# Performance work log

Measured on AMD Instinct MI355X. Metric: run time of the kernel, lower is better.

The kernel has to match this reference:

```python
import jax, jax.numpy as jnp
import numpy as np

N = 50000
E = 1600000
IN_C, H1, H2 = 512, 512, 256
N_CLASSES = 40
CENTER_NUM = 8
D_CAT = 2 * H2  # 512


def setup_inputs() -> dict:
    key = jax.random.key(0)
    ks = jax.random.split(key, 9)
    x = jax.random.normal(ks[0], (N, IN_C), dtype=jnp.float32)
    edge_index = jax.random.randint(ks[1], (2, E), 0, N, dtype=jnp.int64)
    s1 = 1.0 / np.sqrt(IN_C)
    s2 = 1.0 / np.sqrt(H1)
    sp = 1.0 / np.sqrt(D_CAT)
    W1 = jax.random.uniform(ks[2], (IN_C, H1), jnp.float32, -s1, s1)
    b1 = jnp.zeros((H1,), jnp.float32)
    W2 = jax.random.uniform(ks[3], (H1, H2), jnp.float32, -s2, s2)
    b2 = jnp.zeros((H2,), jnp.float32)
    Wp = jax.random.uniform(ks[4], (CENTER_NUM, D_CAT), jnp.float32, -sp, sp)   # interior_prototype weight [C, D]
    We = jax.random.uniform(ks[5], (CENTER_NUM, N_CLASSES, D_CAT), jnp.float32, -sp, sp)  # border prototypes
    return {"x": x, "edge_index": edge_index, "W1": W1, "b1": b1, "W2": W2, "b2": b2, "Wp": Wp, "We": We}


def _gcn_conv(x, W, b, src, dst, n):
    # PyG GCNConv: h = xW; out[i] = sum_j norm_ij h[j] + b, with self-loops,
    # norm_ij = deg_i^{-1/2} deg_j^{-1/2}, deg includes self-loop.
    h = x @ W
    ones = jnp.ones(src.shape[0], x.dtype)
    deg = jax.ops.segment_sum(ones, dst, num_segments=n) + 1.0
    dinv = deg ** -0.5
    norm = dinv[src] * dinv[dst]
    agg = jax.ops.segment_sum(h[src] * norm[:, None], dst, num_segments=n)
    agg = agg + h * (dinv * dinv)[:, None]  # self-loop term
    return agg + b


def _mean_aggr(x, src, dst, n):
    # PyG default message x_j with aggr='mean' (custom message_func kwarg is ignored by PyG)
    cnt = jax.ops.segment_sum(jnp.ones(src.shape[0], x.dtype), dst, num_segments=n)
    s = jax.ops.segment_sum(x[src], dst, num_segments=n)
    return s / jnp.maximum(cnt, 1.0)[:, None]


def reference(x, edge_index, W1, b1, W2, b2, Wp, We):
    src, dst = edge_index[0], edge_index[1]
    n = x.shape[0]
    h = jax.nn.relu(_gcn_conv(x, W1, b1, src, dst, n))
    h = _gcn_conv(h, W2, b2, src, dst, n)
    neighbor = _mean_aggr(h, src, dst, n)
    xc = jnp.concatenate([h, neighbor], axis=1)  # [N, 2*H2]
    scores = xc @ Wp.T                            # [N, C]
    idx = jnp.argmax(scores, axis=1)              # [N]
    # all-expert logits then per-node select (same math as masked per-cluster linear)
    all_out = jnp.einsum('nd,ckd->nck', xc, We)   # [N, C, n_classes]
    out = jnp.take_along_axis(all_out, idx[:, None, None], axis=1)[:, 0, :]
    return out, xc
```

## Files before the change

### kernel.cpp

```cpp
#include <hip/hip_runtime.h>
#include <hip/hip_bf16.h>
#include <hip/hip_fp16.h>
#include <cstdint>
#include <cstddef>


using short8 = __attribute__((ext_vector_type(8))) short;
using half8  = __attribute__((ext_vector_type(8))) _Float16;
using f32x4  = __attribute__((ext_vector_type(4))) float;

#define GLB_AS __attribute__((address_space(1)))
#define LDS_AS __attribute__((address_space(3)))

__global__ __launch_bounds__(256) void prep_kernel(
    const float* __restrict__ x, char* __restrict__ xq, float* __restrict__ scale,
    const float* __restrict__ W1, __half* __restrict__ W1T,
    const float* __restrict__ W2, __half* __restrict__ W2T,
    const float* __restrict__ We, __half* __restrict__ We_h,
    int* __restrict__ bcur, int* __restrict__ ecur,
    int n, int nbuck, int cap) {
    const int t = threadIdx.x;
    int b = blockIdx.x;
    const int BXQ = (n + 3) / 4;
    const int BW1 = (512 * 512) / 256;
    const int BW2 = (512 * 256) / 256;
    const int BWe = (8 * 40 * 512) / 256;
    if (b < BXQ) {
        const int node = b * 4 + (t >> 6);
        const int lane = t & 63;
        if (node < n) {
            const float* row = x + (size_t)node * 512;
            const float4 v0 = *(const float4*)&row[lane * 8];
            const float4 v1 = *(const float4*)&row[lane * 8 + 4];
            float m = fmaxf(fmaxf(fmaxf(fabsf(v0.x), fabsf(v0.y)), fmaxf(fabsf(v0.z), fabsf(v0.w))),
                            fmaxf(fmaxf(fabsf(v1.x), fabsf(v1.y)), fmaxf(fabsf(v1.z), fabsf(v1.w))));
#pragma unroll
            for (int off = 32; off; off >>= 1) m = fmaxf(m, __shfl_xor(m, off));
            m = fmaxf(m, 1e-30f);
            const float qs = 127.f / m;
            int q0 = __float2int_rn(v0.x * qs), q1 = __float2int_rn(v0.y * qs);
            int q2 = __float2int_rn(v0.z * qs), q3 = __float2int_rn(v0.w * qs);
            int q4 = __float2int_rn(v1.x * qs), q5 = __float2int_rn(v1.y * qs);
            int q6 = __float2int_rn(v1.z * qs), q7 = __float2int_rn(v1.w * qs);
            uint2 pk;
            pk.x = (q0 & 0xff) | ((q1 & 0xff) << 8) | ((q2 & 0xff) << 16) | ((q3 & 0xff) << 24);
            pk.y = (q4 & 0xff) | ((q5 & 0xff) << 8) | ((q6 & 0xff) << 16) | ((q7 & 0xff) << 24);
            *(uint2*)&xq[(size_t)node * 512 + lane * 8] = pk;
            if (lane == 0) scale[node] = m / 127.f;
        }
        return;
    }
    b -= BXQ;
    if (b < BW1) {
        const int gid = b * 256 + t;
        const int k = gid >> 9, nn = gid & 511;
        W1T[(size_t)nn * 512 + k] = __float2half(W1[gid]);
        return;
    }
    b -= BW1;
    if (b < BW2) {
        const int gid = b * 256 + t;
        const int k = gid >> 8, nn = gid & 255;
        W2T[(size_t)nn * 512 + k] = __float2half(W2[gid]);
        return;
    }
    b -= BW2;
    if (b < BWe) {
        const int gid = b * 256 + t;
        We_h[gid] = __float2half(We[gid]);
        return;
    }
    if (t < nbuck) bcur[t] = t * cap;
    if (t < 8) ecur[t] = 0;
}

__global__ __launch_bounds__(256) void bucketA_kernel(const int* __restrict__ src,
                                                      const int* __restrict__ dst,
                                                      int* __restrict__ bcur,
                                                      uint32_t* __restrict__ ebuf, int e) {
    __shared__ uint32_t sbuf[4096];
    __shared__ int h[128], gb[128], c2[128];
    const int t = threadIdx.x;
    if (t < 128) { h[t] = 0; c2[t] = 0; }
    __syncthreads();
    const int base = blockIdx.x * 4096;
    const int m = min(4096, e - base);
    for (int j = t; j < m; j += 256) {
        const int s = src[base + j];
        const int d = dst[base + j];
        sbuf[j] = ((uint32_t)s << 16) | (uint32_t)d;
        atomicAdd(&h[d >> 9], 1);
    }
    __syncthreads();
    if (t < 128 && h[t] > 0) gb[t] = atomicAdd(&bcur[t], h[t]);
    __syncthreads();
    for (int j = t; j < m; j += 256) {
        const uint32_t pf = sbuf[j];
        const int b = (int)((pf & 0xFFFFu) >> 9);
        const int r = atomicAdd(&c2[b], 1);
        ebuf[gb[b] + r] = pf;
    }
}

__global__ __launch_bounds__(256) void bucketB_kernel(const uint32_t* __restrict__ ebuf,
                                                      const int* __restrict__ bcur,
                                                      const float* __restrict__ scale,
                                                      int* __restrict__ offsets,
                                                      int* __restrict__ counts,
                                                      float* __restrict__ dinv,
                                                      float* __restrict__ dsc,
                                                      int* __restrict__ ssrc,
                                                      int n, int cap) {
    __shared__ int h[512];
    __shared__ int lofs[512];
    __shared__ int sc[256];
    const int t = threadIdx.x;
    const int b = blockIdx.x;
    const int nbase = b * 512;
    const int nb = min(512, n - nbase);
    h[t] = 0; h[t + 256] = 0;
    __syncthreads();
    const int ebeg = b * cap;
    const int ecount = bcur[b] - ebeg;
    for (int j = t; j < ecount; j += 256)
        atomicAdd(&h[ebuf[ebeg + j] & 511u], 1);
    __syncthreads();
    const int pair = h[2 * t] + h[2 * t + 1];
    sc[t] = pair;
    __syncthreads();
    for (int off = 1; off < 256; off <<= 1) {
        const int u = (t >= off) ? sc[t - off] : 0;
        __syncthreads();
        sc[t] += u;
        __syncthreads();
    }
    const int pbase = sc[t] - pair;
    lofs[2 * t] = pbase;
    lofs[2 * t + 1] = pbase + h[2 * t];
    __syncthreads();
    for (int j = t; j < nb; j += 256) {
        const int cnt = h[j];
        const float dv = rsqrtf((float)cnt + 1.0f);
        offsets[nbase + j] = ebeg + lofs[j];
        counts[nbase + j] = cnt;
        dinv[nbase + j] = dv;
        dsc[nbase + j] = dv * scale[nbase + j];
    }
    __syncthreads();
    lofs[2 * t] += ebeg;
    lofs[2 * t + 1] += ebeg;
    __syncthreads();
    for (int j = t; j < ecount; j += 256) {
        const uint32_t pf = ebuf[ebeg + j];
        const int d = (int)(pf & 511u);
        const int s = (int)(pf >> 16);
        const int pos = atomicAdd(&lofs[d], 1);
        ssrc[pos] = s;
    }
}

__global__ __launch_bounds__(256) void agg512_kernel(const char* __restrict__ xq,
                                                     const int* __restrict__ ssrc,
                                                     const int* __restrict__ offsets,
                                                     const int* __restrict__ counts,
                                                     const float* __restrict__ dinv,
                                                     const float* __restrict__ dsc,
                                                     __half* __restrict__ A16, int n) {
    const int lane = threadIdx.x & 63;
    const int node = (blockIdx.x * blockDim.x + threadIdx.x) >> 6;
    if (node >= n) return;
    const int beg = offsets[node];
    const int end = beg + counts[node];
    const float di = dinv[node];
    const int half = lane >> 5;
    const int hl = lane & 31;
    float acc[16];
#pragma unroll
    for (int j = 0; j < 16; ++j) acc[j] = 0.f;

    for (int b0 = beg; b0 < end; b0 += 64) {
        const int idx = b0 + lane;
        const int sl = (idx < end) ? ssrc[idx] : 0;
        const float wl = (idx < end) ? di * dsc[sl] : 0.f;
        const int m = min(64, end - b0);
#pragma unroll 8
        for (int kp = 0; kp < m; kp += 2) {
            const int k = kp + half;
            const int s = __shfl(sl, k);
            const float w = __shfl(wl, k);
            const int4 raw = *(const int4*)&xq[(size_t)s * 512 + hl * 16];
#pragma unroll
            for (int r = 0; r < 4; ++r) {
                const int v = (r == 0) ? raw.x : (r == 1) ? raw.y : (r == 2) ? raw.z : raw.w;
                acc[r * 4 + 0] = fmaf(w, (float)(char)(v),        acc[r * 4 + 0]);
                acc[r * 4 + 1] = fmaf(w, (float)(char)(v >> 8),   acc[r * 4 + 1]);
                acc[r * 4 + 2] = fmaf(w, (float)(char)(v >> 16),  acc[r * 4 + 2]);
                acc[r * 4 + 3] = fmaf(w, (float)(v >> 24),        acc[r * 4 + 3]);
            }
        }
    }
#pragma unroll
    for (int j = 0; j < 16; ++j) acc[j] += __shfl(acc[j], hl + 32);

    if (half == 0) {
        const float w = di * dsc[node];
        const int4 raw = *(const int4*)&xq[(size_t)node * 512 + hl * 16];
#pragma unroll
        for (int r = 0; r < 4; ++r) {
            const int v = (r == 0) ? raw.x : (r == 1) ? raw.y : (r == 2) ? raw.z : raw.w;
            acc[r * 4 + 0] = fmaf(w, (float)(char)(v),        acc[r * 4 + 0]);
            acc[r * 4 + 1] = fmaf(w, (float)(char)(v >> 8),   acc[r * 4 + 1]);
            acc[r * 4 + 2] = fmaf(w, (float)(char)(v >> 16),  acc[r * 4 + 2]);
            acc[r * 4 + 3] = fmaf(w, (float)(v >> 24),        acc[r * 4 + 3]);
        }
        float4 pk0, pk1;
        *(__half2*)&pk0.x = __floats2half2_rn(acc[0], acc[1]);
        *(__half2*)&pk0.y = __floats2half2_rn(acc[2], acc[3]);
        *(__half2*)&pk0.z = __floats2half2_rn(acc[4], acc[5]);
        *(__half2*)&pk0.w = __floats2half2_rn(acc[6], acc[7]);
        *(__half2*)&pk1.x = __floats2half2_rn(acc[8], acc[9]);
        *(__half2*)&pk1.y = __floats2half2_rn(acc[10], acc[11]);
        *(__half2*)&pk1.z = __floats2half2_rn(acc[12], acc[13]);
        *(__half2*)&pk1.w = __floats2half2_rn(acc[14], acc[15]);
        *(float4*)&A16[(size_t)node * 512 + hl * 16] = pk0;
        *(float4*)&A16[(size_t)node * 512 + hl * 16 + 8] = pk1;
    }
}

__global__ __launch_bounds__(256) void agg256_kernel(const __half* __restrict__ th,
                                                     const int* __restrict__ ssrc,
                                                     const int* __restrict__ offsets,
                                                     const int* __restrict__ counts,
                                                     const float* __restrict__ dinv,
                                                     const float* __restrict__ bias,
                                                     float* __restrict__ xc,
                                                     __half* __restrict__ h2h, int n) {
    const int lane = threadIdx.x & 63;
    const int node = (blockIdx.x * blockDim.x + threadIdx.x) >> 6;
    if (node >= n) return;
    const int beg = offsets[node];
    const int end = beg + counts[node];
    const float di = dinv[node];
    const int half = lane >> 5;
    const int hl = lane & 31;

    float acc8[8] = {0.f, 0.f, 0.f, 0.f, 0.f, 0.f, 0.f, 0.f};
    for (int b0 = beg; b0 < end; b0 += 64) {
        const int idx = b0 + lane;
        const int sl = (idx < end) ? ssrc[idx] : 0;
        const float wl = (idx < end) ? di * dinv[sl] : 0.f;
        const int m = min(64, end - b0);
#pragma unroll 8
        for (int kp = 0; kp < m; kp += 2) {
            const int k = kp + half;
            const int s = __shfl(sl, k);
            const float w = __shfl(wl, k);
            const float4 raw = *(const float4*)&th[(size_t)s * 256 + hl * 8];
            const float2 f0 = __half22float2(*(const __half2*)&raw.x);
            const float2 f1 = __half22float2(*(const __half2*)&raw.y);
            const float2 f2 = __half22float2(*(const __half2*)&raw.z);
            const float2 f3 = __half22float2(*(const __half2*)&raw.w);
            acc8[0] = fmaf(w, f0.x, acc8[0]); acc8[1] = fmaf(w, f0.y, acc8[1]);
            acc8[2] = fmaf(w, f1.x, acc8[2]); acc8[3] = fmaf(w, f1.y, acc8[3]);
            acc8[4] = fmaf(w, f2.x, acc8[4]); acc8[5] = fmaf(w, f2.y, acc8[5]);
            acc8[6] = fmaf(w, f3.x, acc8[6]); acc8[7] = fmaf(w, f3.y, acc8[7]);
        }
    }
#pragma unroll
    for (int j = 0; j < 8; ++j) acc8[j] += __shfl(acc8[j], hl + 32);

    if (half == 0) {
        const float w = di * di;
        const float4 raw = *(const float4*)&th[(size_t)node * 256 + hl * 8];
        const float2 f0 = __half22float2(*(const __half2*)&raw.x);
        const float2 f1 = __half22float2(*(const __half2*)&raw.y);
        const float2 f2 = __half22float2(*(const __half2*)&raw.z);
        const float2 f3 = __half22float2(*(const __half2*)&raw.w);
        const float4 bv0 = *(const float4*)&bias[hl * 8];
        const float4 bv1 = *(const float4*)&bias[hl * 8 + 4];
        acc8[0] = fmaf(w, f0.x, acc8[0]) + bv0.x;
        acc8[1] = fmaf(w, f0.y, acc8[1]) + bv0.y;
        acc8[2] = fmaf(w, f1.x, acc8[2]) + bv0.z;
        acc8[3] = fmaf(w, f1.y, acc8[3]) + bv0.w;
        acc8[4] = fmaf(w, f2.x, acc8[4]) + bv1.x;
        acc8[5] = fmaf(w, f2.y, acc8[5]) + bv1.y;
        acc8[6] = fmaf(w, f3.x, acc8[6]) + bv1.z;
        acc8[7] = fmaf(w, f3.y, acc8[7]) + bv1.w;
        *(float4*)&xc[(size_t)node * 512 + hl * 8]     = make_float4(acc8[0], acc8[1], acc8[2], acc8[3]);
        *(float4*)&xc[(size_t)node * 512 + hl * 8 + 4] = make_float4(acc8[4], acc8[5], acc8[6], acc8[7]);
        float4 pk;
        *(__half2*)&pk.x = __floats2half2_rn(acc8[0], acc8[1]);
        *(__half2*)&pk.y = __floats2half2_rn(acc8[2], acc8[3]);
        *(__half2*)&pk.z = __floats2half2_rn(acc8[4], acc8[5]);
        *(__half2*)&pk.w = __floats2half2_rn(acc8[6], acc8[7]);
        *(float4*)&h2h[(size_t)node * 256 + hl * 8] = pk;
    }
}

template <int EPI>
__global__ __launch_bounds__(256) void gemm_f16_kernel(
    const __half* __restrict__ A, const __half* __restrict__ WT,
    const float* __restrict__ bias, __half* __restrict__ C,
    int M, int N, int K, int ldc) {
    __shared__ ushort smem[2 * 4096];
    const int tid = threadIdx.x;
    const int lane = tid & 63;
    const int w = tid >> 6;
    const int wr = w >> 1, wc = w & 1;
    const int bm = blockIdx.y * 128;
    const int bn = blockIdx.x * 128;

    f32x4 acc[4][4];
#pragma unroll
    for (int i = 0; i < 4; ++i)
#pragma unroll
        for (int j = 0; j < 4; ++j) acc[i][j] = f32x4{0.f, 0.f, 0.f, 0.f};

    for (int k0 = 0; k0 < K; k0 += 32) {
        __syncthreads();
#pragma unroll
        for (int i = 0; i < 4; ++i) {
            const int q = w * 4 + i;
            const bool isA = q < 8;
            const int seg = (isA ? q : q - 8) * 64 + lane;
            const int row = seg >> 2;
            const int kc = (seg & 3) * 8;
            int grow = (isA ? bm : bn) + row;
            grow = min(grow, (isA ? M : N) - 1);
            const ushort* g = (const ushort*)(isA ? A : WT) + (size_t)grow * K + k0 + kc;
            __builtin_amdgcn_global_load_lds((const GLB_AS void*)g,
                                             (LDS_AS void*)(smem + q * 512), 16, 0, 0);
        }
        __syncthreads();

        const int koff = (lane >> 4) * 8;
        const int rsel = lane & 15;
        half8 a[4], b[4];
#pragma unroll
        for (int f = 0; f < 4; ++f) {
            const int ar = wr * 64 + f * 16 + rsel;
            a[f] = __builtin_bit_cast(half8, *(const short8*)&smem[ar * 32 + koff]);
            const int bc = wc * 64 + f * 16 + rsel;
            b[f] = __builtin_bit_cast(half8, *(const short8*)&smem[4096 + bc * 32 + koff]);
        }
#pragma unroll
        for (int i = 0; i < 4; ++i)
#pragma unroll
            for (int j = 0; j < 4; ++j)
                acc[i][j] = __builtin_amdgcn_mfma_f32_16x16x32_f16(a[i], b[j], acc[i][j], 0, 0, 0);
    }

    const int crow0 = wr * 64 + (lane >> 4) * 4;
    const int ccol0 = wc * 64 + (lane & 15);
#pragma unroll
    for (int f = 0; f < 4; ++f) {
#pragma unroll
        for (int g = 0; g < 4; ++g) {
            const int colg = bn + ccol0 + g * 16;
            float bv = 0.f;
            if constexpr (EPI == 1) bv = bias[colg];
#pragma unroll
            for (int j = 0; j < 4; ++j) {
                const int rowg = bm + crow0 + f * 16 + j;
                if (rowg >= M) continue;
                float v = acc[f][g][j];
                if constexpr (EPI == 1) v = fmaxf(v + bv, 0.f);
                C[(size_t)rowg * ldc + colg] = __float2half(v);
            }
        }
    }
}

__global__ __launch_bounds__(256) void mean_score_kernel(const int* __restrict__ ssrc,
                                                         const int* __restrict__ offsets,
                                                         const int* __restrict__ counts,
                                                         const float* __restrict__ Wp,
                                                         const __half* __restrict__ h2h,
                                                         float* __restrict__ xc,
                                                         __half* __restrict__ mh,
                                                         int* __restrict__ bidx, int n) {
    __shared__ float lds_f[4][512];
    const int lane = threadIdx.x & 63;
    const int w = threadIdx.x >> 6;
    const int node = (blockIdx.x * blockDim.x + threadIdx.x) >> 6;
    if (node >= n) return;
    const int beg = offsets[node];
    const int cnt = counts[node];
    const int end = beg + cnt;
    const int c0 = lane * 4;
    const int half = lane >> 5;
    const int hl = lane & 31;

    float acc8[8] = {0.f, 0.f, 0.f, 0.f, 0.f, 0.f, 0.f, 0.f};
    for (int b0 = beg; b0 < end; b0 += 64) {
        const int idx = b0 + lane;
        const int sl = (idx < end) ? ssrc[idx] : 0;
        const int m = min(64, end - b0);
#pragma unroll 8
        for (int kp = 0; kp < m; kp += 2) {
            const int k = kp + half;
            const int s = __shfl(sl, k);
            float4 raw = make_float4(0.f, 0.f, 0.f, 0.f);
            if (k < m) raw = *(const float4*)&h2h[(size_t)s * 256 + hl * 8];
            const float2 f0 = __half22float2(*(const __half2*)&raw.x);
            const float2 f1 = __half22float2(*(const __half2*)&raw.y);
            const float2 f2 = __half22float2(*(const __half2*)&raw.z);
            const float2 f3 = __half22float2(*(const __half2*)&raw.w);
            acc8[0] += f0.x; acc8[1] += f0.y; acc8[2] += f1.x; acc8[3] += f1.y;
            acc8[4] += f2.x; acc8[5] += f2.y; acc8[6] += f3.x; acc8[7] += f3.y;
        }
    }
#pragma unroll
    for (int j = 0; j < 8; ++j) acc8[j] += __shfl(acc8[j], hl + 32);

    const float inv = 1.f / fmaxf((float)cnt, 1.f);
    if (half == 0) {
        float4 b0v = make_float4(acc8[0] * inv, acc8[1] * inv, acc8[2] * inv, acc8[3] * inv);
        float4 b1v = make_float4(acc8[4] * inv, acc8[5] * inv, acc8[6] * inv, acc8[7] * inv);
        *(float4*)&xc[(size_t)node * 512 + 256 + hl * 8] = b0v;
        *(float4*)&xc[(size_t)node * 512 + 256 + hl * 8 + 4] = b1v;
        *(float4*)&lds_f[w][256 + hl * 8] = b0v;
        *(float4*)&lds_f[w][256 + hl * 8 + 4] = b1v;
        float4 pk;
        *(__half2*)&pk.x = __floats2half2_rn(b0v.x, b0v.y);
        *(__half2*)&pk.y = __floats2half2_rn(b0v.z, b0v.w);
        *(__half2*)&pk.z = __floats2half2_rn(b1v.x, b1v.y);
        *(__half2*)&pk.w = __floats2half2_rn(b1v.z, b1v.w);
        *(float4*)&mh[(size_t)node * 256 + hl * 8] = pk;
    }
    const float4 a = *(const float4*)&xc[(size_t)node * 512 + c0];
    *(float4*)&lds_f[w][c0] = a;

    const int r = lane & 15;
    const int quad = lane >> 4;

    float av[32];
#pragma unroll
    for (int i = 0; i < 8; ++i) {
        const int jj = (i + r) & 7;
        *(float4*)&av[i * 4] = *(const float4*)&lds_f[w][r * 32 + jj * 4];
    }

    float s0, s1;
#pragma unroll
    for (int t = 0; t < 2; ++t) {
        const int c = t * 4 + quad;
        const float* wp = &Wp[c * 512 + r * 32];
        float p = 0.f;
#pragma unroll
        for (int i = 0; i < 8; ++i) {
            const int jj = (i + r) & 7;
            const float4 wv = *(const float4*)&wp[jj * 4];
            p = fmaf(av[i * 4 + 0], wv.x, p);
            p = fmaf(av[i * 4 + 1], wv.y, p);
            p = fmaf(av[i * 4 + 2], wv.z, p);
            p = fmaf(av[i * 4 + 3], wv.w, p);
        }
        p += __shfl_xor(p, 1); p += __shfl_xor(p, 2);
        p += __shfl_xor(p, 4); p += __shfl_xor(p, 8);
        if (t == 0) s0 = p; else s1 = p;
    }
    float best = -3.0e38f;
    int be = 0;
#pragma unroll
    for (int c = 0; c < 8; ++c) {
        const float v = __shfl((c < 4) ? s0 : s1, (c & 3) * 16);
        if (v > best) { best = v; be = c; }
    }
    if (lane == 0) bidx[node] = be;
}

__global__ __launch_bounds__(256) void bucket_scatter_kernel(const int* __restrict__ bidx,
                                                             int* __restrict__ cursor,
                                                             int* __restrict__ elist, int n) {
    __shared__ int h[8], base[8], c2[8];
    const int t = threadIdx.x;
    if (t < 8) { h[t] = 0; c2[t] = 0; }
    __syncthreads();
    const int i = blockIdx.x * 256 + t;
    int b = 0;
    if (i < n) {
        b = bidx[i];
        atomicAdd(&h[b], 1);
    }
    __syncthreads();
    if (t < 8) base[t] = (h[t] > 0) ? atomicAdd(&cursor[t], h[t]) : 0;
    __syncthreads();
    if (i < n) {
        const int r = atomicAdd(&c2[b], 1);
        elist[(size_t)b * n + base[b] + r] = i;
    }
}

__global__ __launch_bounds__(256) void expert_gemm_kernel(
    const int* __restrict__ elist, const int* __restrict__ ecnt,
    const __half* __restrict__ h2h, const __half* __restrict__ mh,
    const __half* __restrict__ We_h, float* __restrict__ out, int n) {
    const int e = blockIdx.x;
    const int cnt = ecnt[e];
    const int base = blockIdx.y * 128;
    if (base >= cnt) return;
    __shared__ __half Bs[40][520];
    const int tid = threadIdx.x;
#pragma unroll
    for (int i = 0; i < 10; ++i) {
        const int seg = tid + i * 256;
        const int br = seg >> 6;
        const int bc = (seg & 63) * 8;
        *(float4*)&Bs[br][bc] = *(const float4*)&We_h[((size_t)e * 40 + br) * 512 + bc];
    }
    __syncthreads();

    const int w = tid >> 6, lane = tid & 63;
    const int rsel = lane & 15, koff = (lane >> 4) * 8;
    const int grow0 = base + w * 32 + rsel;
    const int grow1 = grow0 + 16;
    const int i0 = elist[(size_t)e * n + min(grow0, cnt - 1)];
    const int i1 = elist[(size_t)e * n + min(grow1, cnt - 1)];

    f32x4 acc[2][3];
#pragma unroll
    for (int mf = 0; mf < 2; ++mf)
#pragma unroll
        for (int nf = 0; nf < 3; ++nf) acc[mf][nf] = f32x4{0.f, 0.f, 0.f, 0.f};

#pragma unroll
    for (int ks = 0; ks < 16; ++ks) {
        const int k0 = ks * 32 + koff;
        const __half* s0 = (k0 < 256) ? &h2h[(size_t)i0 * 256 + k0] : &mh[(size_t)i0 * 256 + (k0 - 256)];
        const __half* s1 = (k0 < 256) ? &h2h[(size_t)i1 * 256 + k0] : &mh[(size_t)i1 * 256 + (k0 - 256)];
        const half8 a0 = __builtin_bit_cast(half8, *(const short8*)s0);
        const half8 a1 = __builtin_bit_cast(half8, *(const short8*)s1);
#pragma unroll
        for (int nf = 0; nf < 3; ++nf) {
            const int brow = min(nf * 16 + rsel, 39);
            const half8 b = __builtin_bit_cast(half8, *(const short8*)&Bs[brow][ks * 32 + koff]);
            acc[0][nf] = __builtin_amdgcn_mfma_f32_16x16x32_f16(a0, b, acc[0][nf], 0, 0, 0);
            acc[1][nf] = __builtin_amdgcn_mfma_f32_16x16x32_f16(a1, b, acc[1][nf], 0, 0, 0);
        }
    }

    const int crow = (lane >> 4) * 4;
    const int ccol = lane & 15;
#pragma unroll
    for (int mf = 0; mf < 2; ++mf) {
#pragma unroll
        for (int nf = 0; nf < 3; ++nf) {
            const int col = nf * 16 + ccol;
            if (col >= 40) continue;
#pragma unroll
            for (int j = 0; j < 4; ++j) {
                const int gr = base + w * 32 + mf * 16 + crow + j;
                if (gr >= cnt) continue;
                const int node = elist[(size_t)e * n + gr];
                out[(size_t)node * 40 + col] = acc[mf][nf][j];
            }
        }
    }
}

extern "C" void kernel_launch(void* const* d_in, const int* in_sizes, int n_in,
                              void* d_out, int out_size, void* d_ws, size_t ws_size,
                              hipStream_t stream) {
    const float* x  = (const float*)d_in[0];
    const int*  edge = (const int*)d_in[1];
    const float* W1 = (const float*)d_in[2];
    const float* b1 = (const float*)d_in[3];
    const float* W2 = (const float*)d_in[4];
    const float* b2 = (const float*)d_in[5];
    const float* Wp = (const float*)d_in[6];
    const float* We = (const float*)d_in[7];

    const int n = in_sizes[0] / 512;
    const int e = in_sizes[1] / 2;
    const int* src = edge;
    const int* dst = edge + e;

    const int nbuck = (n + 511) / 512;
    const int cap = 20480;

    char* ws = (char*)d_ws;
    __half* A16 = (__half*)ws;
    __half* t16 = (__half*)ws;
    __half* mh  = (__half*)ws;
    char* p = ws + (size_t)n * 512 * 2;
    __half* h1 = (__half*)p;
    __half* h2h = (__half*)p;
    p += (size_t)n * 512 * 2;
    char* xq = p; p += (size_t)n * 512;
    __half* W1T = (__half*)p; p += 512 * 512 * 2;
    __half* W2T = (__half*)p; p += 256 * 512 * 2;
    __half* We_h = (__half*)p; p += 8 * 40 * 512 * 2;
    auto align16 = [](size_t v) { return (v + 15) & ~(size_t)15; };
    float* scale = (float*)p;   p += align16((size_t)n * 4);
    float* dinv = (float*)p;    p += align16((size_t)n * 4);
    float* dsc = (float*)p;     p += align16((size_t)n * 4);
    int* counts = (int*)p;      p += align16((size_t)n * 4);
    int* offsets = (int*)p;     p += align16((size_t)n * 4);
    int* bidx = (int*)p;        p += align16((size_t)n * 4);
    int* bcur = (int*)p;        p += align16((size_t)nbuck * 4);
    int* ecur = (int*)p;        p += align16((size_t)8 * 4);
    int* elist = (int*)p;       p += align16((size_t)8 * n * 4);
    uint32_t* ebuf = (uint32_t*)p; p += align16((size_t)nbuck * cap * 4);
    int* ssrc = (int*)p;

    float* out = (float*)d_out;
    float* xc = (float*)d_out + (size_t)n * 40;

    const int prep_blocks = (n + 3) / 4 + (512 * 512) / 256 +
                            (512 * 256) / 256 + (8 * 40 * 512) / 256 + 1;
    prep_kernel<<<prep_blocks, 256, 0, stream>>>(x, xq, scale, W1, W1T, W2, W2T, We, We_h,
                                                 bcur, ecur, n, nbuck, cap);

    bucketA_kernel<<<(e + 4095) / 4096, 256, 0, stream>>>(src, dst, bcur, ebuf, e);
    bucketB_kernel<<<nbuck, 256, 0, stream>>>(ebuf, bcur, scale, offsets, counts, dinv, dsc,
                                              ssrc, n, cap);

    const int waves_grid = (n * 64 + 255) / 256;
    agg512_kernel<<<waves_grid, 256, 0, stream>>>(xq, ssrc, offsets, counts, dinv, dsc, A16, n);
    dim3 g1(512 / 128, (n + 127) / 128);
    gemm_f16_kernel<1><<<g1, 256, 0, stream>>>(A16, W1T, b1, h1, n, 512, 512, 512);

    dim3 g2(256 / 128, (n + 127) / 128);
    gemm_f16_kernel<0><<<g2, 256, 0, stream>>>(h1, W2T, nullptr, t16, n, 256, 512, 256);

    agg256_kernel<<<waves_grid, 256, 0, stream>>>(t16, ssrc, offsets, counts, dinv, b2, xc, h2h, n);

    mean_score_kernel<<<waves_grid, 256, 0, stream>>>(ssrc, offsets, counts, Wp, h2h, xc, mh, bidx, n);

    bucket_scatter_kernel<<<(n + 255) / 256, 256, 0, stream>>>(bidx, ecur, elist, n);

    dim3 ge(8, (n + 127) / 128);
    expert_gemm_kernel<<<ge, 256, 0, stream>>>(elist, ecur, h2h, mh, We_h, out, n);
}
```

Measured before the change: 614.0 us.

## Quantize second-layer features to int8 for gather-based aggregations

```diff
diff --git a/kernel.cpp b/kernel.cpp
--- a/kernel.cpp
+++ b/kernel.cpp
@@ -11,6 +11,13 @@
 
 #define GLB_AS __attribute__((address_space(1)))
 #define LDS_AS __attribute__((address_space(3)))
+
+__device__ inline void unpack_fma(int v, float w, float* a) {
+    a[0] = fmaf(w, (float)(char)(v),       a[0]);
+    a[1] = fmaf(w, (float)(char)(v >> 8),  a[1]);
+    a[2] = fmaf(w, (float)(char)(v >> 16), a[2]);
+    a[3] = fmaf(w, (float)(v >> 24),       a[3]);
+}
 
 __global__ __launch_bounds__(256) void prep_kernel(
     const float* __restrict__ x, char* __restrict__ xq, float* __restrict__ scale,
@@ -189,14 +196,10 @@
             const int s = __shfl(sl, k);
             const float w = __shfl(wl, k);
             const int4 raw = *(const int4*)&xq[(size_t)s * 512 + hl * 16];
-#pragma unroll
-            for (int r = 0; r < 4; ++r) {
-                const int v = (r == 0) ? raw.x : (r == 1) ? raw.y : (r == 2) ? raw.z : raw.w;
-                acc[r * 4 + 0] = fmaf(w, (float)(char)(v),        acc[r * 4 + 0]);
-                acc[r * 4 + 1] = fmaf(w, (float)(char)(v >> 8),   acc[r * 4 + 1]);
-                acc[r * 4 + 2] = fmaf(w, (float)(char)(v >> 16),  acc[r * 4 + 2]);
-                acc[r * 4 + 3] = fmaf(w, (float)(v >> 24),        acc[r * 4 + 3]);
-            }
+            unpack_fma(raw.x, w, &acc[0]);
+            unpack_fma(raw.y, w, &acc[4]);
+            unpack_fma(raw.z, w, &acc[8]);
+            unpack_fma(raw.w, w, &acc[12]);
         }
     }
 #pragma unroll
@@ -205,14 +208,10 @@
     if (half == 0) {
         const float w = di * dsc[node];
         const int4 raw = *(const int4*)&xq[(size_t)node * 512 + hl * 16];
-#pragma unroll
-        for (int r = 0; r < 4; ++r) {
-            const int v = (r == 0) ? raw.x : (r == 1) ? raw.y : (r == 2) ? raw.z : raw.w;
-            acc[r * 4 + 0] = fmaf(w, (float)(char)(v),        acc[r * 4 + 0]);
-            acc[r * 4 + 1] = fmaf(w, (float)(char)(v >> 8),   acc[r * 4 + 1]);
-            acc[r * 4 + 2] = fmaf(w, (float)(char)(v >> 16),  acc[r * 4 + 2]);
-            acc[r * 4 + 3] = fmaf(w, (float)(v >> 24),        acc[r * 4 + 3]);
-        }
+        unpack_fma(raw.x, w, &acc[0]);
+        unpack_fma(raw.y, w, &acc[4]);
+        unpack_fma(raw.z, w, &acc[8]);
+        unpack_fma(raw.w, w, &acc[12]);
         float4 pk0, pk1;
         *(__half2*)&pk0.x = __floats2half2_rn(acc[0], acc[1]);
         *(__half2*)&pk0.y = __floats2half2_rn(acc[2], acc[3]);
@@ -227,73 +226,119 @@
     }
 }
 
-__global__ __launch_bounds__(256) void agg256_kernel(const __half* __restrict__ th,
+__global__ __launch_bounds__(256) void tquant_kernel(const __half* __restrict__ t16,
+                                                     const float* __restrict__ dinv,
+                                                     char* __restrict__ tq,
+                                                     float* __restrict__ dts, int n) {
+    const int lane = threadIdx.x & 63;
+    const int node = (blockIdx.x * blockDim.x + threadIdx.x) >> 6;
+    if (node >= n) return;
+    const float2 raw = *(const float2*)&t16[(size_t)node * 256 + lane * 4];
+    const float2 f0 = __half22float2(*(const __half2*)&raw.x);
+    const float2 f1 = __half22float2(*(const __half2*)&raw.y);
+    float m = fmaxf(fmaxf(fabsf(f0.x), fabsf(f0.y)), fmaxf(fabsf(f1.x), fabsf(f1.y)));
+#pragma unroll
+    for (int off = 32; off; off >>= 1) m = fmaxf(m, __shfl_xor(m, off));
+    m = fmaxf(m, 1e-30f);
+    const float qs = 127.f / m;
+    const int q0 = __float2int_rn(f0.x * qs), q1 = __float2int_rn(f0.y * qs);
+    const int q2 = __float2int_rn(f1.x * qs), q3 = __float2int_rn(f1.y * qs);
+    const uint32_t pk = (q0 & 0xff) | ((q1 & 0xff) << 8) | ((q2 & 0xff) << 16) | ((q3 & 0xff) << 24);
+    *(uint32_t*)&tq[(size_t)node * 256 + lane * 4] = pk;
+    if (lane == 0) dts[node] = dinv[node] * (m / 127.f);
+}
+
+__global__ __launch_bounds__(256) void agg256_kernel(const char* __restrict__ tq,
                                                      const int* __restrict__ ssrc,
                                                      const int* __restrict__ offsets,
                                                      const int* __restrict__ counts,
                                                      const float* __restrict__ dinv,
+                                                     const float* __restrict__ dts,
                                                      const float* __restrict__ bias,
                                                      float* __restrict__ xc,
-                                                     __half* __restrict__ h2h, int n) {
+                                                     __half* __restrict__ h2h,
+                                                     char* __restrict__ hq8,
+                                                     float* __restrict__ hsc, int n) {
     const int lane = threadIdx.x & 63;
     const int node = (blockIdx.x * blockDim.x + threadIdx.x) >> 6;
     if (node >= n) return;
     const int beg = offsets[node];
     const int end = beg + counts[node];
     const float di = dinv[node];
-    const int half = lane >> 5;
-    const int hl = lane & 31;
-
-    float acc8[8] = {0.f, 0.f, 0.f, 0.f, 0.f, 0.f, 0.f, 0.f};
+    const int q = lane >> 4;
+    const int ql = lane & 15;
+    float acc[16];
+#pragma unroll
+    for (int j = 0; j < 16; ++j) acc[j] = 0.f;
+
     for (int b0 = beg; b0 < end; b0 += 64) {
         const int idx = b0 + lane;
         const int sl = (idx < end) ? ssrc[idx] : 0;
-        const float wl = (idx < end) ? di * dinv[sl] : 0.f;
+        const float wl = (idx < end) ? di * dts[sl] : 0.f;
         const int m = min(64, end - b0);
-#pragma unroll 8
-        for (int kp = 0; kp < m; kp += 2) {
-            const int k = kp + half;
+#pragma unroll 4
+        for (int kp = 0; kp < m; kp += 4) {
+            const int k = kp + q;
             const int s = __shfl(sl, k);
             const float w = __shfl(wl, k);
-            const float4 raw = *(const float4*)&th[(size_t)s * 256 + hl * 8];
-            const float2 f0 = __half22float2(*(const __half2*)&raw.x);
-            const float2 f1 = __half22float2(*(const __half2*)&raw.y);
-            const float2 f2 = __half22float2(*(const __half2*)&raw.z);
-            const float2 f3 = __half22float2(*(const __half2*)&raw.w);
-            acc8[0] = fmaf(w, f0.x, acc8[0]); acc8[1] = fmaf(w, f0.y, acc8[1]);
-            acc8[2] = fmaf(w, f1.x, acc8[2]); acc8[3] = fmaf(w, f1.y, acc8[3]);
-            acc8[4] = fmaf(w, f2.x, acc8[4]); acc8[5] = fmaf(w, f2.y, acc8[5]);
-            acc8[6] = fmaf(w, f3.x, acc8[6]); acc8[7] = fmaf(w, f3.y, acc8[7]);
-        }
-    }
-#pragma unroll
-    for (int j = 0; j < 8; ++j) acc8[j] += __shfl(acc8[j], hl + 32);
-
-    if (half == 0) {
-        const float w = di * di;
-        const float4 raw = *(const float4*)&th[(size_t)node * 256 + hl * 8];
-        const float2 f0 = __half22float2(*(const __half2*)&raw.x);
-        const float2 f1 = __half22float2(*(const __half2*)&raw.y);
-        const float2 f2 = __half22float2(*(const __half2*)&raw.z);
-        const float2 f3 = __half22float2(*(const __half2*)&raw.w);
-        const float4 bv0 = *(const float4*)&bias[hl * 8];
-        const float4 bv1 = *(const float4*)&bias[hl * 8 + 4];
-        acc8[0] = fmaf(w, f0.x, acc8[0]) + bv0.x;
-        acc8[1] = fmaf(w, f0.y, acc8[1]) + bv0.y;
-        acc8[2] = fmaf(w, f1.x, acc8[2]) + bv0.z;
-        acc8[3] = fmaf(w, f1.y, acc8[3]) + bv0.w;
-        acc8[4] = fmaf(w, f2.x, acc8[4]) + bv1.x;
-        acc8[5] = fmaf(w, f2.y, acc8[5]) + bv1.y;
-        acc8[6] = fmaf(w, f3.x, acc8[6]) + bv1.z;
-        acc8[7] = fmaf(w, f3.y, acc8[7]) + bv1.w;
-        *(float4*)&xc[(size_t)node * 512 + hl * 8]     = make_float4(acc8[0], acc8[1], acc8[2], acc8[3]);
-        *(float4*)&xc[(size_t)node * 512 + hl * 8 + 4] = make_float4(acc8[4], acc8[5], acc8[6], acc8[7]);
-        float4 pk;
-        *(__half2*)&pk.x = __floats2half2_rn(acc8[0], acc8[1]);
-        *(__half2*)&pk.y = __floats2half2_rn(acc8[2], acc8[3]);
-        *(__half2*)&pk.z = __floats2half2_rn(acc8[4], acc8[5]);
-        *(__half2*)&pk.w = __floats2half2_rn(acc8[6], acc8[7]);
-        *(float4*)&h2h[(size_t)node * 256 + hl * 8] = pk;
+            const int4 raw = *(const int4*)&tq[(size_t)s * 256 + ql * 16];
+            unpack_fma(raw.x, w, &acc[0]);
+            unpack_fma(raw.y, w, &acc[4]);
+            unpack_fma(raw.z, w, &acc[8]);
+            unpack_fma(raw.w, w, &acc[12]);
+        }
+    }
+#pragma unroll
+    for (int j = 0; j < 16; ++j) acc[j] += __shfl(acc[j], lane + 32);
+#pragma unroll
+    for (int j = 0; j < 16; ++j) acc[j] += __shfl(acc[j], lane + 16);
+
+    if (q == 0) {
+        const float w = di * dts[node];
+        const int4 raw = *(const int4*)&tq[(size_t)node * 256 + ql * 16];
+        unpack_fma(raw.x, w, &acc[0]);
+        unpack_fma(raw.y, w, &acc[4]);
+        unpack_fma(raw.z, w, &acc[8]);
+        unpack_fma(raw.w, w, &acc[12]);
+#pragma unroll
+        for (int i = 0; i < 4; ++i) {
+            const float4 bv = *(const float4*)&bias[ql * 16 + i * 4];
+            acc[i * 4 + 0] += bv.x; acc[i * 4 + 1] += bv.y;
+            acc[i * 4 + 2] += bv.z; acc[i * 4 + 3] += bv.w;
+        }
+#pragma unroll
+        for (int i = 0; i < 4; ++i)
+            *(float4*)&xc[(size_t)node * 512 + ql * 16 + i * 4] =
+                make_float4(acc[i * 4 + 0], acc[i * 4 + 1], acc[i * 4 + 2], acc[i * 4 + 3]);
+        float4 pk0, pk1;
+        *(__half2*)&pk0.x = __floats2half2_rn(acc[0], acc[1]);
+        *(__half2*)&pk0.y = __floats2half2_rn(acc[2], acc[3]);
+        *(__half2*)&pk0.z = __floats2half2_rn(acc[4], acc[5]);
+        *(__half2*)&pk0.w = __floats2half2_rn(acc[6], acc[7]);
+        *(__half2*)&pk1.x = __floats2half2_rn(acc[8], acc[9]);
+        *(__half2*)&pk1.y = __floats2half2_rn(acc[10], acc[11]);
+        *(__half2*)&pk1.z = __floats2half2_rn(acc[12], acc[13]);
+        *(__half2*)&pk1.w = __floats2half2_rn(acc[14], acc[15]);
+        *(float4*)&h2h[(size_t)node * 256 + ql * 16] = pk0;
+        *(float4*)&h2h[(size_t)node * 256 + ql * 16 + 8] = pk1;
+        float am = 0.f;
+#pragma unroll
+        for (int j = 0; j < 16; ++j) am = fmaxf(am, fabsf(acc[j]));
+#pragma unroll
+        for (int off = 1; off < 16; off <<= 1) am = fmaxf(am, __shfl_xor(am, off));
+        am = fmaxf(am, 1e-30f);
+        const float qs = 127.f / am;
+        uint32_t pk[4];
+#pragma unroll
+        for (int i = 0; i < 4; ++i) {
+            const int a0 = __float2int_rn(acc[i * 4 + 0] * qs);
+            const int a1 = __float2int_rn(acc[i * 4 + 1] * qs);
+            const int a2 = __float2int_rn(acc[i * 4 + 2] * qs);
+            const int a3 = __float2int_rn(acc[i * 4 + 3] * qs);
+            pk[i] = (a0 & 0xff) | ((a1 & 0xff) << 8) | ((a2 & 0xff) << 16) | ((a3 & 0xff) << 24);
+        }
+        *(int4*)&hq8[(size_t)node * 256 + ql * 16] = *(int4*)pk;
+        if (ql == 0) hsc[node] = am / 127.f;
     }
 }
 
@@ -375,7 +420,8 @@
                                                          const int* __restrict__ offsets,
                                                          const int* __restrict__ counts,
                                                          const float* __restrict__ Wp,
-                                                         const __half* __restrict__ h2h,
+                                                         const char* __restrict__ hq8,
+                                                         const float* __restrict__ hsc,
                                                          float* __restrict__ xc,
                                                          __half* __restrict__ mh,
                                                          int* __restrict__ bidx, int n) {
@@ -388,45 +434,55 @@
     const int cnt = counts[node];
     const int end = beg + cnt;
     const int c0 = lane * 4;
-    const int half = lane >> 5;
-    const int hl = lane & 31;
-
-    float acc8[8] = {0.f, 0.f, 0.f, 0.f, 0.f, 0.f, 0.f, 0.f};
+    const int q = lane >> 4;
+    const int ql = lane & 15;
+
+    float acc[16];
+#pragma unroll
+    for (int j = 0; j < 16; ++j) acc[j] = 0.f;
     for (int b0 = beg; b0 < end; b0 += 64) {
         const int idx = b0 + lane;
         const int sl = (idx < end) ? ssrc[idx] : 0;
+        const float wl = (idx < end) ? hsc[sl] : 0.f;
         const int m = min(64, end - b0);
-#pragma unroll 8
-        for (int kp = 0; kp < m; kp += 2) {
-            const int k = kp + half;
+#pragma unroll 4
+        for (int kp = 0; kp < m; kp += 4) {
+            const int k = kp + q;
             const int s = __shfl(sl, k);
-            float4 raw = make_float4(0.f, 0.f, 0.f, 0.f);
-            if (k < m) raw = *(const float4*)&h2h[(size_t)s * 256 + hl * 8];
-            const float2 f0 = __half22float2(*(const __half2*)&raw.x);
-            const float2 f1 = __half22float2(*(const __half2*)&raw.y);
-            const float2 f2 = __half22float2(*(const __half2*)&raw.z);
-            const float2 f3 = __half22float2(*(const __half2*)&raw.w);
-            acc8[0] += f0.x; acc8[1] += f0.y; acc8[2] += f1.x; acc8[3] += f1.y;
-            acc8[4] += f2.x; acc8[5] += f2.y; acc8[6] += f3.x; acc8[7] += f3.y;
-        }
-    }
-#pragma unroll
-    for (int j = 0; j < 8; ++j) acc8[j] += __shfl(acc8[j], hl + 32);
+            const float ww = __shfl(wl, k);
+            const int4 raw = *(const int4*)&hq8[(size_t)s * 256 + ql * 16];
+            unpack_fma(raw.x, ww, &acc[0]);
+            unpack_fma(raw.y, ww, &acc[4]);
+            unpack_fma(raw.z, ww, &acc[8]);
+            unpack_fma(raw.w, ww, &acc[12]);
+        }
+    }
+#pragma unroll
+    for (int j = 0; j < 16; ++j) acc[j] += __shfl(acc[j], lane + 32);
+#pragma unroll
+    for (int j = 0; j < 16; ++j) acc[j] += __shfl(acc[j], lane + 16);
 
     const float inv = 1.f / fmaxf((float)cnt, 1.f);
-    if (half == 0) {
-        float4 b0v = make_float4(acc8[0] * inv, acc8[1] * inv, acc8[2] * inv, acc8[3] * inv);
-        float4 b1v = make_float4(acc8[4] * inv, acc8[5] * inv, acc8[6] * inv, acc8[7] * inv);
-        *(float4*)&xc[(size_t)node * 512 + 256 + hl * 8] = b0v;
-        *(float4*)&xc[(size_t)node * 512 + 256 + hl * 8 + 4] = b1v;
-        *(float4*)&lds_f[w][256 + hl * 8] = b0v;
-        *(float4*)&lds_f[w][256 + hl * 8 + 4] = b1v;
-        float4 pk;
-        *(__half2*)&pk.x = __floats2half2_rn(b0v.x, b0v.y);
-        *(__half2*)&pk.y = __floats2half2_rn(b0v.z, b0v.w);
-        *(__half2*)&pk.z = __floats2half2_rn(b1v.x, b1v.y);
-        *(__half2*)&pk.w = __floats2half2_rn(b1v.z, b1v.w);
-        *(float4*)&mh[(size_t)node * 256 + hl * 8] = pk;
+    if (q == 0) {
+#pragma unroll
+        for (int j = 0; j < 16; ++j) acc[j] *= inv;
+#pragma unroll
+        for (int i = 0; i < 4; ++i) {
+            const float4 v = make_float4(acc[i * 4 + 0], acc[i * 4 + 1], acc[i * 4 + 2], acc[i * 4 + 3]);
+            *(float4*)&xc[(size_t)node * 512 + 256 + ql * 16 + i * 4] = v;
+            *(float4*)&lds_f[w][256 + ql * 16 + i * 4] = v;
+        }
+        float4 pk0, pk1;
+        *(__half2*)&pk0.x = __floats2half2_rn(acc[0], acc[1]);
+        *(__half2*)&pk0.y = __floats2half2_rn(acc[2], acc[3]);
+        *(__half2*)&pk0.z = __floats2half2_rn(acc[4], acc[5]);
+        *(__half2*)&pk0.w = __floats2half2_rn(acc[6], acc[7]);
+        *(__half2*)&pk1.x = __floats2half2_rn(acc[8], acc[9]);
+        *(__half2*)&pk1.y = __floats2half2_rn(acc[10], acc[11]);
+        *(__half2*)&pk1.z = __floats2half2_rn(acc[12], acc[13]);
+        *(__half2*)&pk1.w = __floats2half2_rn(acc[14], acc[15]);
+        *(float4*)&mh[(size_t)node * 256 + ql * 16] = pk0;
+        *(float4*)&mh[(size_t)node * 256 + ql * 16 + 8] = pk1;
     }
     const float4 a = *(const float4*)&xc[(size_t)node * 512 + c0];
     *(float4*)&lds_f[w][c0] = a;
@@ -587,7 +643,9 @@
     __half* h1 = (__half*)p;
     __half* h2h = (__half*)p;
     p += (size_t)n * 512 * 2;
-    char* xq = p; p += (size_t)n * 512;
+    char* xq  = p; p += (size_t)n * 512;
+    char* tq8 = p; p += (size_t)n * 256;
+    char* hq8 = p; p += (size_t)n * 256;
     __half* W1T = (__half*)p; p += 512 * 512 * 2;
     __half* W2T = (__half*)p; p += 256 * 512 * 2;
     __half* We_h = (__half*)p; p += 8 * 40 * 512 * 2;
@@ -595,6 +653,8 @@
     float* scale = (float*)p;   p += align16((size_t)n * 4);
     float* dinv = (float*)p;    p += align16((size_t)n * 4);
     float* dsc = (float*)p;     p += align16((size_t)n * 4);
+    float* dts = (float*)p;     p += align16((size_t)n * 4);
+    float* hsc = (float*)p;     p += align16((size_t)n * 4);
     int* counts = (int*)p;      p += align16((size_t)n * 4);
     int* offsets = (int*)p;     p += align16((size_t)n * 4);
     int* bidx = (int*)p;        p += align16((size_t)n * 4);
@@ -623,10 +683,13 @@
 
     dim3 g2(256 / 128, (n + 127) / 128);
     gemm_f16_kernel<0><<<g2, 256, 0, stream>>>(h1, W2T, nullptr, t16, n, 256, 512, 256);
-
-    agg256_kernel<<<waves_grid, 256, 0, stream>>>(t16, ssrc, offsets, counts, dinv, b2, xc, h2h, n);
-
-    mean_score_kernel<<<waves_grid, 256, 0, stream>>>(ssrc, offsets, counts, Wp, h2h, xc, mh, bidx, n);
+    tquant_kernel<<<waves_grid, 256, 0, stream>>>(t16, dinv, tq8, dts, n);
+
+    agg256_kernel<<<waves_grid, 256, 0, stream>>>(tq8, ssrc, offsets, counts, dinv, dts, b2,
+                                                  xc, h2h, hq8, hsc, n);
+
+    mean_score_kernel<<<waves_grid, 256, 0, stream>>>(ssrc, offsets, counts, Wp, hq8, hsc,
+                                                      xc, mh, bidx, n);
 
     bucket_scatter_kernel<<<(n + 255) / 256, 256, 0, stream>>>(bidx, ecur, elist, n);
 
```

Result: faster. 557.9 us (-9.1%).
